# Kernel tuning notes

Measured on AMD Instinct MI355X. Metric: run time of the kernel, lower is better.

Reference implementation:

```python
import jax, jax.numpy as jnp
import numpy as np

M, K, N = 32, 8192, 8192      # tokens, infeatures, outfeatures
GROUP = 128                   # quantization group size along K
PACK = 8                      # 32 bits / 4 bits per value


def _dequant(qweight, scales):
    """Unpack int4 nibbles (packed 8-per-int32 along K) and apply per-group
    symmetric dequant: w = (q - 8) * scale, matching Marlin's fused dequant."""
    kp, n = qweight.shape  # (K//8, N)
    shifts = (4 * jnp.arange(PACK, dtype=jnp.int32))[None, :, None]
    q = ((qweight[:, None, :] >> shifts) & 15)          # (K//8, 8, N)
    q = q.reshape(kp * PACK, n).astype(jnp.float32)     # (K, N)
    groups = scales.shape[0]
    gsz = (kp * PACK) // groups
    w = (q.reshape(groups, gsz, n) - 8.0) * scales[:, None, :]
    return w.reshape(kp * PACK, n)                      # (K, N) fp


def setup_inputs() -> dict:
    key = jax.random.key(0)
    kA, kQ, kS, kB = jax.random.split(key, 4)
    A = jax.random.normal(kA, (M, K), jnp.float32)
    # draw raw 4-bit codes then pack 8 of them into each int32 along K
    q4 = jax.random.randint(kQ, (K, N), 0, 16, jnp.int32)
    shifts = (4 * jnp.arange(PACK, dtype=jnp.int32))[None, :, None]
    qweight = jnp.sum(q4.reshape(K // PACK, PACK, N) << shifts, axis=1).astype(jnp.int32)
    scales = jax.random.uniform(kS, (K // GROUP, N), jnp.float32, 0.005, 0.02)
    bias = jax.random.normal(kB, (N,), jnp.float32) * 0.01
    return {"A": A, "qweight": qweight, "scales": scales, "bias": bias}


def reference(A, qweight, scales, bias):
    # Marlin mul(A, B, C, s) computes C = A @ dequant(B, s); then + bias
    W = _dequant(qweight, scales)          # (K, N)
    return A @ W + bias                    # (M, N)
```

## Files before the change

### kernel.cpp

```cpp
#include <hip/hip_runtime.h>
#include <hip/hip_bf16.h>
#include <stdint.h>

#define M_DIM 32
#define K_DIM 8192
#define N_DIM 8192
#define NGROUPS 64
#define KSPLIT 8
#define KPART (K_DIM / KSPLIT)
#define GPART (NGROUPS / KSPLIT)
#define BN 64

typedef __attribute__((ext_vector_type(8))) short short8;
typedef __attribute__((ext_vector_type(4))) float floatx4;

#define AS1(p) ((const __attribute__((address_space(1))) void*)(p))
#define AS3(p) ((__attribute__((address_space(3))) void*)(p))

__global__ void marlin_prep_kernel(const float* __restrict__ A,
                                   uint16_t* __restrict__ Abf,
                                   float* __restrict__ R,
                                   float4* __restrict__ out4) {
    const int m = blockIdx.x;
    const int qtr = blockIdx.y;
    const int t = threadIdx.x;
    const int octet = qtr * 256 + t;
    const int k0 = octet * 8;

    {
        const int gtid = (qtr * 32 + m) * 256 + t;
        const float4 z = make_float4(0.f, 0.f, 0.f, 0.f);
        out4[gtid * 2] = z;
        out4[gtid * 2 + 1] = z;
    }

    const float* a = A + m * K_DIM + k0;
    uint16_t b[8];
    float sum = 0.f;
#pragma unroll
    for (int j = 0; j < 8; j++) {
        union { __hip_bfloat16 h; uint16_t u; } cv;
        cv.h = __float2bfloat16(a[j]);
        b[j] = cv.u;
        sum += __bfloat162float(cv.h);
    }
    uint32_t w0 = (uint32_t)b[0] | ((uint32_t)b[4] << 16);
    uint32_t w1 = (uint32_t)b[1] | ((uint32_t)b[5] << 16);
    uint32_t w2 = (uint32_t)b[2] | ((uint32_t)b[6] << 16);
    uint32_t w3 = (uint32_t)b[3] | ((uint32_t)b[7] << 16);
    *(uint4*)(Abf + (size_t)m * K_DIM + k0) = make_uint4(w0, w1, w2, w3);

#pragma unroll
    for (int off = 1; off < 16; off <<= 1) sum += __shfl_xor(sum, off, 16);
    if ((t & 15) == 0) R[m * NGROUPS + qtr * 16 + (t >> 4)] = sum;
}

__global__ __launch_bounds__(512, 4) void
MarlinQuantLinear_68556267979256_kernel(const int* __restrict__ qw,
                                        const float* __restrict__ scales,
                                        const float* __restrict__ bias,
                                        const uint16_t* __restrict__ Abf,
                                        const float* __restrict__ R,
                                        float* __restrict__ out) {
    __shared__ uint32_t qbuf[2][16 * 64];
    __shared__ uint32_t abuf[2][32 * 64];
    __shared__ float    r_lds[32 * 9];

    const int bx = blockIdx.x;
    const int bz = blockIdx.y;
    const int nbase = bx * BN;
    const int kbase = bz * KPART;
    const int gbase = bz * GPART;
    const int qrow0 = bz * (KPART / 8);

    const int tid = threadIdx.x;
    const int w = tid >> 6;
    const int lane = tid & 63;
    const int quad = lane >> 4;
    const int l16 = lane & 15;
    const int mtile = w & 1;
    const int ntile = w >> 1;
    const int ncol = nbase + ntile * 16 + l16;
    const int arow = mtile * 16 + l16;

    if (tid < 256) {
        const int mm = tid >> 3, gg = tid & 7;
        r_lds[mm * 9 + gg] = 136.0f * R[mm * NGROUPS + gbase + gg];
    }

    const float* scol = scales + (size_t)gbase * N_DIM + ncol;
    float s[GPART];
#pragma unroll
    for (int g = 0; g < GPART; g++) s[g] = scol[g * N_DIM];

    const int sra = tid >> 4, spa = tid & 15;
    const uint16_t* ga_base = Abf + (size_t)sra * K_DIM + kbase
                            + ((spa ^ (sra & 15)) << 3);
    const int srq = tid >> 4, spq = tid & 15;
    const int* gq_base = qw + (size_t)(qrow0 + srq) * N_DIM + nbase
                       + ((spq * 4) ^ ((srq & 1) << 4));

    auto stage = [&](int g, int buf) {
        __builtin_amdgcn_global_load_lds(AS1(ga_base + g * 128),
                                         AS3(&abuf[buf][w * 256]), 16, 0, 0);
        if (tid < 256)
            __builtin_amdgcn_global_load_lds(AS1(gq_base + (size_t)g * 16 * N_DIM),
                                             AS3(&qbuf[buf][w * 256]), 16, 0, 0);
    };

    stage(0, 0);

    floatx4 C = {0.f, 0.f, 0.f, 0.f};

#pragma unroll
    for (int g = 0; g < GPART; g++) {
        __syncthreads();
        if (g + 1 < GPART) stage(g + 1, (g + 1) & 1);

        const uint32_t* qb = qbuf[g & 1];
        const uint32_t* ab = abuf[g & 1];
        floatx4 accg = {0.f, 0.f, 0.f, 0.f};
#pragma unroll
        for (int t = 0; t < 4; t++) {
            const uint32_t q =
                qb[(t * 4 + quad) * 64 + ((ntile * 16 + l16) ^ ((quad & 1) << 4))];
            union { uint32_t u[4]; short8 v; } fb;
            fb.u[0] = ( q        & 0x000F000Fu) | 0x43004300u;
            fb.u[1] = ((q >> 4)  & 0x000F000Fu) | 0x43004300u;
            fb.u[2] = ((q >> 8)  & 0x000F000Fu) | 0x43004300u;
            fb.u[3] = ((q >> 12) & 0x000F000Fu) | 0x43004300u;
            const short8 fa = *(const short8*)
                &ab[arow * 64 + (((t * 4 + quad) ^ (arow & 15)) << 2)];
            accg = __builtin_amdgcn_mfma_f32_16x16x32_bf16(fa, fb.v, accg, 0, 0, 0);
        }
#pragma unroll
        for (int r = 0; r < 4; r++) {
            const float tval = accg[r] - r_lds[(mtile * 16 + quad * 4 + r) * 9 + g];
            C[r] = fmaf(s[g], tval, C[r]);
        }
    }

    const float bv = (bz == 0) ? bias[ncol] : 0.0f;
#pragma unroll
    for (int r = 0; r < 4; r++) {
        const int m = mtile * 16 + quad * 4 + r;
        atomicAdd(&out[(size_t)m * N_DIM + ncol], C[r] + bv);
    }
}

extern "C" void kernel_launch(void* const* d_in, const int* in_sizes, int n_in,
                              void* d_out, int out_size, void* d_ws, size_t ws_size,
                              hipStream_t stream) {
    const float* A      = (const float*)d_in[0];
    const int*   qw     = (const int*)d_in[1];
    const float* scales = (const float*)d_in[2];
    const float* bias   = (const float*)d_in[3];
    float* out = (float*)d_out;

    uint16_t* Abf = (uint16_t*)d_ws;
    float*    R   = (float*)((char*)d_ws + (size_t)M_DIM * K_DIM * 2);

    marlin_prep_kernel<<<dim3(M_DIM, 4), 256, 0, stream>>>(A, Abf, R, (float4*)out);
    MarlinQuantLinear_68556267979256_kernel<<<dim3(N_DIM / BN, KSPLIT), 512, 0, stream>>>(
        qw, scales, bias, Abf, R, out);
}
```

Baseline: 92.38 us.

## Widen N tile to 128 with two MFMA tiles per wave and split K 16 ways

Doubles the block's N width so each wave computes two 16-column output tiles and reuses one A fragment across two MFMAs. K-split rises from 8 to 16, so each block handles 4 groups and the grid keeps 1024 blocks. All 512 threads now stage the weight tile instead of half. The intent is to raise A reuse and balance staging work. In exchange, atomic adds into the output double (16 partial sums per element) and the group pipeline per block gets shorter.

```diff
diff --git a/kernel.cpp b/kernel.cpp
--- a/kernel.cpp
+++ b/kernel.cpp
@@ -6,10 +6,10 @@
 #define K_DIM 8192
 #define N_DIM 8192
 #define NGROUPS 64
-#define KSPLIT 8
+#define KSPLIT 16
 #define KPART (K_DIM / KSPLIT)
 #define GPART (NGROUPS / KSPLIT)
-#define BN 64
+#define BN 128
 
 typedef __attribute__((ext_vector_type(8))) short short8;
 typedef __attribute__((ext_vector_type(4))) float floatx4;
@@ -62,9 +62,9 @@
                                         const uint16_t* __restrict__ Abf,
                                         const float* __restrict__ R,
                                         float* __restrict__ out) {
-    __shared__ uint32_t qbuf[2][16 * 64];
+    __shared__ uint32_t qbuf[2][16 * 128];
     __shared__ uint32_t abuf[2][32 * 64];
-    __shared__ float    r_lds[32 * 9];
+    __shared__ float    r_lds[32 * 5];
 
     const int bx = blockIdx.x;
     const int bz = blockIdx.y;
@@ -79,38 +79,42 @@
     const int quad = lane >> 4;
     const int l16 = lane & 15;
     const int mtile = w & 1;
-    const int ntile = w >> 1;
-    const int ncol = nbase + ntile * 16 + l16;
+    const int nt0 = (w >> 1) * 2;
+    const int ncol0 = nbase + nt0 * 16 + l16;
+    const int ncol1 = ncol0 + 16;
     const int arow = mtile * 16 + l16;
 
-    if (tid < 256) {
-        const int mm = tid >> 3, gg = tid & 7;
-        r_lds[mm * 9 + gg] = 136.0f * R[mm * NGROUPS + gbase + gg];
+    if (tid < 128) {
+        const int mm = tid >> 2, gg = tid & 3;
+        r_lds[mm * 5 + gg] = 136.0f * R[mm * NGROUPS + gbase + gg];
     }
 
-    const float* scol = scales + (size_t)gbase * N_DIM + ncol;
-    float s[GPART];
+    const float* scol = scales + (size_t)gbase * N_DIM;
+    float s0[GPART], s1[GPART];
 #pragma unroll
-    for (int g = 0; g < GPART; g++) s[g] = scol[g * N_DIM];
+    for (int g = 0; g < GPART; g++) {
+        s0[g] = scol[g * N_DIM + ncol0];
+        s1[g] = scol[g * N_DIM + ncol1];
+    }
 
     const int sra = tid >> 4, spa = tid & 15;
     const uint16_t* ga_base = Abf + (size_t)sra * K_DIM + kbase
                             + ((spa ^ (sra & 15)) << 3);
-    const int srq = tid >> 4, spq = tid & 15;
+    const int srq = tid >> 5, spq = tid & 31;
     const int* gq_base = qw + (size_t)(qrow0 + srq) * N_DIM + nbase
                        + ((spq * 4) ^ ((srq & 1) << 4));
 
     auto stage = [&](int g, int buf) {
         __builtin_amdgcn_global_load_lds(AS1(ga_base + g * 128),
                                          AS3(&abuf[buf][w * 256]), 16, 0, 0);
-        if (tid < 256)
-            __builtin_amdgcn_global_load_lds(AS1(gq_base + (size_t)g * 16 * N_DIM),
-                                             AS3(&qbuf[buf][w * 256]), 16, 0, 0);
+        __builtin_amdgcn_global_load_lds(AS1(gq_base + (size_t)g * 16 * N_DIM),
+                                         AS3(&qbuf[buf][w * 256]), 16, 0, 0);
     };
 
     stage(0, 0);
 
-    floatx4 C = {0.f, 0.f, 0.f, 0.f};
+    floatx4 C0 = {0.f, 0.f, 0.f, 0.f};
+    floatx4 C1 = {0.f, 0.f, 0.f, 0.f};
 
 #pragma unroll
     for (int g = 0; g < GPART; g++) {
@@ -119,32 +123,44 @@
 
         const uint32_t* qb = qbuf[g & 1];
         const uint32_t* ab = abuf[g & 1];
-        floatx4 accg = {0.f, 0.f, 0.f, 0.f};
+        floatx4 acc0 = {0.f, 0.f, 0.f, 0.f};
+        floatx4 acc1 = {0.f, 0.f, 0.f, 0.f};
 #pragma unroll
         for (int t = 0; t < 4; t++) {
-            const uint32_t q =
-                qb[(t * 4 + quad) * 64 + ((ntile * 16 + l16) ^ ((quad & 1) << 4))];
-            union { uint32_t u[4]; short8 v; } fb;
-            fb.u[0] = ( q        & 0x000F000Fu) | 0x43004300u;
-            fb.u[1] = ((q >> 4)  & 0x000F000Fu) | 0x43004300u;
-            fb.u[2] = ((q >> 8)  & 0x000F000Fu) | 0x43004300u;
-            fb.u[3] = ((q >> 12) & 0x000F000Fu) | 0x43004300u;
+            const int qrow = (t * 4 + quad) * 128;
+            const uint32_t qA =
+                qb[qrow + ((nt0 * 16 + l16) ^ ((quad & 1) << 4))];
+            const uint32_t qB =
+                qb[qrow + (((nt0 + 1) * 16 + l16) ^ ((quad & 1) << 4))];
             const short8 fa = *(const short8*)
                 &ab[arow * 64 + (((t * 4 + quad) ^ (arow & 15)) << 2)];
-            accg = __builtin_amdgcn_mfma_f32_16x16x32_bf16(fa, fb.v, accg, 0, 0, 0);
+            union { uint32_t u[4]; short8 v; } fb;
+            fb.u[0] = ( qA        & 0x000F000Fu) | 0x43004300u;
+            fb.u[1] = ((qA >> 4)  & 0x000F000Fu) | 0x43004300u;
+            fb.u[2] = ((qA >> 8)  & 0x000F000Fu) | 0x43004300u;
+            fb.u[3] = ((qA >> 12) & 0x000F000Fu) | 0x43004300u;
+            acc0 = __builtin_amdgcn_mfma_f32_16x16x32_bf16(fa, fb.v, acc0, 0, 0, 0);
+            fb.u[0] = ( qB        & 0x000F000Fu) | 0x43004300u;
+            fb.u[1] = ((qB >> 4)  & 0x000F000Fu) | 0x43004300u;
+            fb.u[2] = ((qB >> 8)  & 0x000F000Fu) | 0x43004300u;
+            fb.u[3] = ((qB >> 12) & 0x000F000Fu) | 0x43004300u;
+            acc1 = __builtin_amdgcn_mfma_f32_16x16x32_bf16(fa, fb.v, acc1, 0, 0, 0);
         }
 #pragma unroll
         for (int r = 0; r < 4; r++) {
-            const float tval = accg[r] - r_lds[(mtile * 16 + quad * 4 + r) * 9 + g];
-            C[r] = fmaf(s[g], tval, C[r]);
+            const float Rv = r_lds[(mtile * 16 + quad * 4 + r) * 5 + g];
+            C0[r] = fmaf(s0[g], acc0[r] - Rv, C0[r]);
+            C1[r] = fmaf(s1[g], acc1[r] - Rv, C1[r]);
         }
     }
 
-    const float bv = (bz == 0) ? bias[ncol] : 0.0f;
+    const float bv0 = (bz == 0) ? bias[ncol0] : 0.0f;
+    const float bv1 = (bz == 0) ? bias[ncol1] : 0.0f;
 #pragma unroll
     for (int r = 0; r < 4; r++) {
         const int m = mtile * 16 + quad * 4 + r;
-        atomicAdd(&out[(size_t)m * N_DIM + ncol], C[r] + bv);
+        atomicAdd(&out[(size_t)m * N_DIM + ncol0], C0[r] + bv0);
+        atomicAdd(&out[(size_t)m * N_DIM + ncol1], C1[r] + bv1);
     }
 }
 
```

Measured after the change: 94.26 us. 2.0% more time.
